# Performance work log

Hardware: AMD Instinct MI355X
Metric: run time of the kernel (lower is better)

## Reference

```python
import jax, jax.numpy as jnp
from jax import lax
import numpy as np

D_MODEL = 512
H = 4
DK = 128
DV = 256
DFF = 2048
N_LAYERS = 12
N_LOC = 100  # 10x10 patches

CONV_SPECS = [(8, 3, 3), (16, 8, 3), (32, 16, 3), (32, 32, 3), (64, 32, 3),
              (64, 64, 3), (128, 64, 3), (128, 128, 3), (256, 128, 3), (512, 256, 2)]
RELU_AFTER = [False, True, False, True, True, True, True, True, True, False]


def setup_inputs() -> dict:
    key = jax.random.key(0)
    keys = iter(jax.random.split(key, 64))

    def nrm(shape, scale=0.02):
        return jax.random.normal(next(keys), shape, dtype=jnp.float32) * scale

    inp = {"x": jax.random.normal(next(keys), (1, 3, 200, 200), dtype=jnp.float32)}
    for i, (o, c, k) in enumerate(CONV_SPECS, 1):
        inp[f"cw{i}"] = nrm((o, c, k, k))
        inp[f"cb{i}"] = nrm((o,))
    inp["Wq"] = nrm((N_LAYERS, H, D_MODEL, DK))
    inp["Wk"] = nrm((N_LAYERS, H, D_MODEL, DK))
    inp["Wv"] = nrm((N_LAYERS, H, D_MODEL, DV))
    inp["Wo"] = nrm((N_LAYERS, H * DV, D_MODEL))
    inp["W1"] = nrm((N_LAYERS, D_MODEL, DFF))
    inp["b1"] = nrm((N_LAYERS, DFF))
    inp["W2"] = nrm((N_LAYERS, DFF, D_MODEL))
    inp["b2"] = nrm((N_LAYERS, D_MODEL))
    return inp


def _extract_patches(x):
    # x: [1,3,200,200] -> 100 patches of [3,20,20], index = i*10 + j
    # patch(i,j) = x[:, :, 20j:20(j+1), 20i:20(i+1)]  (i=cols outer, j=rows inner)
    x = x.reshape(3, 10, 20, 10, 20)            # [c, j_blk, row, i_blk, col]
    return jnp.transpose(x, (3, 1, 0, 2, 4)).reshape(N_LOC, 3, 20, 20)


def _local_embed(patches, cws, cbs):
    h = patches  # [100,3,20,20]
    for w, b, r in zip(cws, cbs, RELU_AFTER):
        h = lax.conv_general_dilated(h, w, (1, 1), 'VALID',
                                     dimension_numbers=('NCHW', 'OIHW', 'NCHW'))
        h = h + b[None, :, None, None]
        if r:
            h = jax.nn.relu(h)
    return h.reshape(N_LOC, D_MODEL)  # spatial reduced to 1x1


def _location_embeddings():
    # createLocationEmbedding(i, j) only uses i (the column-block coordinate).
    pos = jnp.repeat(jnp.arange(0, 200, 20, dtype=jnp.float32), 10)  # [100]
    k = jnp.arange(256, dtype=jnp.float32)
    inv = jnp.power(jnp.float32(10000.0), 2.0 * k / 256.0)
    ang = pos[:, None] / inv[None, :]  # [100,256]
    return jnp.concatenate([jnp.sin(ang), jnp.cos(ang)], axis=1)  # [100,512]


def _encoder_layer(h, Wq, Wk, Wv, Wo, W1, b1, W2, b2):
    # Multi-head attention; NOTE: scale uses K.size(0) = n_locations (faithful quirk).
    scale = 1.0 / jnp.sqrt(jnp.float32(N_LOC))
    q = jnp.einsum('nd,hdk->hnk', h, Wq)
    k = jnp.einsum('nd,hdk->hnk', h, Wk)
    v = jnp.einsum('nd,hdv->hnv', h, Wv)
    s = jnp.einsum('hnk,hmk->hnm', q, k) * scale
    a = jax.nn.softmax(s, axis=-1)
    o = jnp.einsum('hnm,hmv->hnv', a, v)
    o = jnp.transpose(o, (1, 0, 2)).reshape(N_LOC, H * DV)
    h = h + o @ Wo
    h = h + (jax.nn.relu(h @ W1 + b1) @ W2 + b2)
    return h


def reference(x, cw1, cb1, cw2, cb2, cw3, cb3, cw4, cb4, cw5, cb5,
              cw6, cb6, cw7, cb7, cw8, cb8, cw9, cb9, cw10, cb10,
              Wq, Wk, Wv, Wo, W1, b1, W2, b2):
    cws = [cw1, cw2, cw3, cw4, cw5, cw6, cw7, cw8, cw9, cw10]
    cbs = [cb1, cb2, cb3, cb4, cb5, cb6, cb7, cb8, cb9, cb10]
    patches = _extract_patches(x)
    h = _local_embed(patches, cws, cbs)
    h = h + _location_embeddings()
    for n in range(N_LAYERS):
        h = _encoder_layer(h, Wq[n], Wk[n], Wv[n], Wo[n], W1[n], b1[n], W2[n], b2[n])
    return h
```

## Files before the change

kernel.cpp:

```cpp
#include <hip/hip_runtime.h>
#include <math.h>

#define NLOC 100

typedef __attribute__((ext_vector_type(8))) _Float16 half8;
typedef __attribute__((ext_vector_type(4))) float f32x4;

#define XP_OFF    0
#define H_OFF     160000
#define QKV_OFF   211200
#define OCAT_OFF  416000
#define FFN_OFF   467200
#define ACTA_OFF  569600
#define ACTB_OFF  889664
#define CWH_OFF   1209728
#define CW1_OFF   1765504
#define WQKVT_OFF 1765824
#define WOT_OFF   8057280
#define W1T_OFF   11203008
#define W2T_OFF   17494464

struct WPack { const float* w[9]; };

__global__ __launch_bounds__(256) void stage_xp(const float* __restrict__ x, float* __restrict__ xp)
{
    int idx = blockIdx.x*256 + threadIdx.x;
    if (idx >= 160000) return;
    int c = idx & 3;
    int idx2 = idx >> 2;
    int p = idx2 / 400;
    int rr = idx2 - p*400;
    int y = rr / 20, xx = rr - y*20;
    int pi = p/10, pj = p - pi*10;
    float v = 0.f;
    if (c < 3) v = x[c*40000 + (pj*20 + y)*200 + pi*20 + xx];
    xp[idx] = v;
}

__global__ __launch_bounds__(256) void cw1repack(const float* __restrict__ w, float* __restrict__ w4)
{
    int idx = threadIdx.x;
    if (idx >= 288) return;
    int c = idx & 3;
    int r = idx >> 2;
    int oc = r / 9, kk = r - oc*9;
    int ky = kk/3, kx = kk - ky*3;
    float v = 0.f;
    if (c < 3) v = w[((oc*3 + c)*3 + ky)*3 + kx];
    w4[idx] = v;
}

__global__ __launch_bounds__(256) void cwrepack(WPack wp, unsigned short* __restrict__ dst)
{
    const int Cin[9]  = {8,16,32,32,64,64,128,128,256};
    const int shift[9]= {3,4,5,5,6,6,7,7,8};
    const int KS[9]   = {3,3,3,3,3,3,3,3,2};
    const int Kpad[9] = {96,160,288,288,576,576,1152,1152,1024};
    const int off[10] = {0,1536,6656,15872,34304,71168,144896,292352,587264,1111552};
    const int total = 1111552;
    for (int i = blockIdx.x*blockDim.x + threadIdx.x; i < total; i += gridDim.x*blockDim.x) {
        int l = 0;
        while (i >= off[l+1]) ++l;
        int rem = i - off[l];
        int kp = Kpad[l];
        int oc = rem / kp;
        int k  = rem - oc*kp;
        int ci = Cin[l];
        int ic = k & (ci - 1);
        int kk = k >> shift[l];
        int ks = KS[l], k2 = ks*ks;
        float v = 0.f;
        if (kk < k2) {
            int ky = kk / ks, kx = kk - ky*ks;
            v = wp.w[l][((oc*ci + ic)*ks + ky)*ks + kx];
        }
        _Float16 hv = (_Float16)v;
        dst[i] = __builtin_bit_cast(unsigned short, hv);
    }
}

__global__ __launch_bounds__(256) void conv1k(const float4* __restrict__ xp4,
    const float4* __restrict__ w4, const float* __restrict__ bias, unsigned short* __restrict__ out)
{
    int idx = blockIdx.x*256 + threadIdx.x;
    if (idx >= 259200) return;
    int oc = idx & 7;
    int r = idx >> 3;
    int p = r / 324;
    int s = r - p*324;
    int sy = s / 18, sx = s - sy*18;
    const float4* ip = xp4 + (size_t)(p*20 + sy)*20 + sx;
    float acc = 0.f;
    #pragma unroll
    for (int ky = 0; ky < 3; ++ky)
        #pragma unroll
        for (int kx = 0; kx < 3; ++kx) {
            float4 iv = ip[ky*20 + kx];
            float4 wv = w4[oc*9 + ky*3 + kx];
            acc += iv.x*wv.x + iv.y*wv.y + iv.z*wv.z;
        }
    acc += bias[oc];
    _Float16 hv = (_Float16)acc;
    out[idx] = __builtin_bit_cast(unsigned short, hv);
}

template<int CIN, int COUT, int KS, int HIN, int WIN, int HOUT, int WOUT, int KPAD, int RELU, int LAST>
__global__ __launch_bounds__(256) void convM(const unsigned short* __restrict__ in,
    const unsigned short* __restrict__ wth, const float* __restrict__ bias,
    unsigned short* __restrict__ out, float* __restrict__ hout)
{
    constexpr int HW = HOUT*WOUT;
    constexpr int M = 100*HW;
    constexpr int MT = (M + 15)/16;
    constexpr int NT = COUT/16;
    int wave = threadIdx.x >> 6, lane = threadIdx.x & 63;
    int t = blockIdx.x*4 + wave;
    if (t >= MT*NT) return;
    int mt = t % MT, nt = t / MT;
    int mrow = lane & 15, quad = lane >> 4;
    int mg = mt*16 + mrow; if (mg >= M) mg = M - 1;
    int p = mg / HW, s = mg - p*HW;
    int sy = s / WOUT, sx = s - sy*WOUT;
    const unsigned short* ap = in + ((size_t)((p*HIN + sy)*WIN + sx))*CIN;
    const unsigned short* bp = wth + ((size_t)(nt*16 + mrow))*KPAD + quad*8;
    f32x4 acc = {0.f, 0.f, 0.f, 0.f};
    #pragma unroll
    for (int k0 = 0; k0 < KPAD; k0 += 32) {
        int k = k0 + quad*8;
        int kk = k / CIN; if (kk > KS*KS - 1) kk = KS*KS - 1;
        int ky = kk / KS, kx = kk - ky*KS;
        uint4 av = *(const uint4*)(ap + (ky*WIN + kx)*CIN + (k & (CIN-1)));
        uint4 bv = *(const uint4*)(bp + k0);
        acc = __builtin_amdgcn_mfma_f32_16x16x32_f16(
            __builtin_bit_cast(half8, av), __builtin_bit_cast(half8, bv), acc, 0, 0, 0);
    }
    int n = nt*16 + mrow;
    float bv = bias[n];
    #pragma unroll
    for (int r = 0; r < 4; ++r) {
        int m = mt*16 + quad*4 + r;
        if (m < M) {
            float v = acc[r] + bv;
            if (RELU) v = fmaxf(v, 0.f);
            if (LAST) {
                int pi = m / 10;
                float pos = 20.f * (float)pi;
                int dd = n & 255;
                float inv = powf(10000.f, (float)dd * (1.f/128.f));
                float ang = pos / inv;
                v += (n < 256) ? sinf(ang) : cosf(ang);
                hout[(size_t)m*512 + n] = v;
            } else {
                _Float16 hv = (_Float16)v;
                out[(size_t)m*COUT + n] = __builtin_bit_cast(unsigned short, hv);
            }
        }
    }
}

__global__ __launch_bounds__(256) void wtrans(
    const float* __restrict__ src, unsigned short* __restrict__ dst,
    int K, int N, int matsPerLayer, int dstLayerStride, int dstBase)
{
    __shared__ float t[32][33];
    int mz = blockIdx.z;
    int layer = mz / matsPerLayer;
    int mi = mz - layer*matsPerLayer;
    const float* s = src + (size_t)mz * K * N;
    unsigned short* d = dst + (size_t)layer*dstLayerStride + dstBase + (size_t)mi * N * K;
    int n0 = blockIdx.x*32, k0 = blockIdx.y*32;
    int tx = threadIdx.x & 31, ty = threadIdx.x >> 5;
    #pragma unroll
    for (int i = 0; i < 32; i += 8) t[ty + i][tx] = s[(size_t)(k0 + ty + i)*N + n0 + tx];
    __syncthreads();
    #pragma unroll
    for (int i = 0; i < 32; i += 8) {
        _Float16 hv = (_Float16)t[tx][ty + i];
        d[(size_t)(n0 + ty + i)*K + k0 + tx] = __builtin_bit_cast(unsigned short, hv);
    }
}

template<int ABITS, int RELU, int ATOMIC, int STOREH>
__global__ __launch_bounds__(256) void gemm16(
    const void* __restrict__ Av, int lda,
    const unsigned short* __restrict__ Bt, int K,
    const float* __restrict__ bias,
    float* __restrict__ C, unsigned short* __restrict__ Ch, int ldc,
    int kchunk)
{
    int lane = threadIdx.x & 63;
    int wave = threadIdx.x >> 6;
    int mrow = lane & 15, quad = lane >> 4;
    int n0 = blockIdx.x*64 + wave*16;
    int m0 = blockIdx.y*16;
    int arow = m0 + mrow; if (arow > 99) arow = 99;
    int k0 = blockIdx.z * kchunk;
    const unsigned short* bp = Bt + (size_t)(n0 + mrow)*K + quad*8 + k0;
    f32x4 acc = {0.f, 0.f, 0.f, 0.f};
    if (ABITS == 16) {
        const unsigned short* ap = (const unsigned short*)Av + (size_t)arow*lda + quad*8 + k0;
        for (int k = 0; k < kchunk; k += 32) {
            uint4 au = *(const uint4*)(ap + k);
            uint4 bu = *(const uint4*)(bp + k);
            acc = __builtin_amdgcn_mfma_f32_16x16x32_f16(
                __builtin_bit_cast(half8, au), __builtin_bit_cast(half8, bu), acc, 0, 0, 0);
        }
    } else {
        const float* ap = (const float*)Av + (size_t)arow*lda + quad*8 + k0;
        for (int k = 0; k < kchunk; k += 32) {
            float4 f0 = *(const float4*)(ap + k);
            float4 f1 = *(const float4*)(ap + k + 4);
            half8 af;
            af[0] = (_Float16)f0.x; af[1] = (_Float16)f0.y;
            af[2] = (_Float16)f0.z; af[3] = (_Float16)f0.w;
            af[4] = (_Float16)f1.x; af[5] = (_Float16)f1.y;
            af[6] = (_Float16)f1.z; af[7] = (_Float16)f1.w;
            uint4 bu = *(const uint4*)(bp + k);
            acc = __builtin_amdgcn_mfma_f32_16x16x32_f16(
                af, __builtin_bit_cast(half8, bu), acc, 0, 0, 0);
        }
    }
    int n = n0 + mrow;
    float bv = (bias != nullptr && blockIdx.z == 0) ? bias[n] : 0.f;
    #pragma unroll
    for (int r = 0; r < 4; ++r) {
        int row = m0 + quad*4 + r;
        if (row < 100) {
            float v = acc[r] + bv;
            if (RELU) v = fmaxf(v, 0.f);
            if (ATOMIC) atomicAdd(&C[(size_t)row*ldc + n], v);
            else if (C != nullptr) C[(size_t)row*ldc + n] = v;
            if (STOREH) {
                _Float16 hv = (_Float16)v;
                Ch[(size_t)row*ldc + n] = __builtin_bit_cast(unsigned short, hv);
            }
        }
    }
}

__global__ __launch_bounds__(256) void attn_kernel(
    const float* __restrict__ qkv, unsigned short* __restrict__ ocat)
{
    __shared__ float qr[128];
    __shared__ float p[100];
    __shared__ float red[2];
    int bx = blockIdx.x;
    int hh = bx / 100, nn = bx - hh*100;
    int t = threadIdx.x;
    if (t < 128) qr[t] = qkv[(size_t)nn*2048 + hh*128 + t];
    __syncthreads();
    float sv = 0.f;
    if (t < 100) {
        const float4* kp = (const float4*)(qkv + (size_t)t*2048 + 512 + hh*128);
        const float4* q4 = (const float4*)qr;
        float s0=0.f, s1=0.f, s2=0.f, s3=0.f;
        #pragma unroll 8
        for (int j = 0; j < 32; ++j) {
            float4 a = q4[j], b = kp[j];
            s0 += a.x*b.x; s1 += a.y*b.y; s2 += a.z*b.z; s3 += a.w*b.w;
        }
        sv = (s0+s1+s2+s3) * 0.1f;
        p[t] = sv;
    }
    __syncthreads();
    if (t < 64) {
        float m = fmaxf(p[t], (t+64 < 100) ? p[t+64] : -1e30f);
        for (int o = 32; o > 0; o >>= 1) m = fmaxf(m, __shfl_down(m, o));
        if (t == 0) red[0] = m;
    }
    __syncthreads();
    float mx = red[0];
    if (t < 100) p[t] = expf(sv - mx);
    __syncthreads();
    if (t < 64) {
        float s = p[t] + ((t+64 < 100) ? p[t+64] : 0.f);
        for (int o = 32; o > 0; o >>= 1) s += __shfl_down(s, o);
        if (t == 0) red[1] = s;
    }
    __syncthreads();
    float inv = 1.0f / red[1];
    const float* vp = qkv + 1024 + hh*256 + t;
    float acc = 0.f;
    #pragma unroll 4
    for (int m = 0; m < 100; ++m) acc += p[m] * vp[(size_t)m*2048];
    _Float16 hv = (_Float16)(acc * inv);
    ocat[(size_t)nn*1024 + hh*256 + t] = __builtin_bit_cast(unsigned short, hv);
}

__global__ __launch_bounds__(256) void copyk(const float* __restrict__ s, float* __restrict__ d, int n)
{
    int i = blockIdx.x*256 + threadIdx.x;
    if (i < n) d[i] = s[i];
}

extern "C" void kernel_launch(void* const* d_in, const int* in_sizes, int n_in,
                              void* d_out, int out_size, void* d_ws, size_t ws_size,
                              hipStream_t stream)
{
    const float* x = (const float*)d_in[0];
    const float* cw1 = (const float*)d_in[1];
    const float* cb[10];
    WPack wpk;
    for (int i = 0; i < 10; ++i) cb[i] = (const float*)d_in[2 + 2*i];
    for (int i = 0; i < 9; ++i)  wpk.w[i] = (const float*)d_in[3 + 2*i];
    const float* Wq = (const float*)d_in[21];
    const float* Wk = (const float*)d_in[22];
    const float* Wv = (const float*)d_in[23];
    const float* Wo = (const float*)d_in[24];
    const float* W1 = (const float*)d_in[25];
    const float* b1 = (const float*)d_in[26];
    const float* W2 = (const float*)d_in[27];
    const float* b2 = (const float*)d_in[28];

    float* ws = (float*)d_ws;
    float* xp  = ws + XP_OFF;
    float* h   = ws + H_OFF;
    float* qkv = ws + QKV_OFF;
    unsigned short* ocat = (unsigned short*)(ws + OCAT_OFF);
    unsigned short* ffn  = (unsigned short*)(ws + FFN_OFF);
    unsigned short* aA   = (unsigned short*)(ws + ACTA_OFF);
    unsigned short* aB   = (unsigned short*)(ws + ACTB_OFF);
    unsigned short* cwh  = (unsigned short*)(ws + CWH_OFF);
    float* cw14 = ws + CW1_OFF;
    unsigned short* wqkvt = (unsigned short*)(ws + WQKVT_OFF);
    unsigned short* wot   = (unsigned short*)(ws + WOT_OFF);
    unsigned short* w1t   = (unsigned short*)(ws + W1T_OFF);
    unsigned short* w2t   = (unsigned short*)(ws + W2T_OFF);

    cw1repack<<<2, 256, 0, stream>>>(cw1, cw14);
    cwrepack<<<2172, 256, 0, stream>>>(wpk, cwh);
    wtrans<<<dim3(4, 16, 48),  256, 0, stream>>>(Wq, wqkvt, 512, 128,  4, 2048*512, 0);
    wtrans<<<dim3(4, 16, 48),  256, 0, stream>>>(Wk, wqkvt, 512, 128,  4, 2048*512, 512*512);
    wtrans<<<dim3(8, 16, 48),  256, 0, stream>>>(Wv, wqkvt, 512, 256,  4, 2048*512, 1024*512);
    wtrans<<<dim3(16, 32, 12), 256, 0, stream>>>(Wo, wot,  1024, 512,  1, 512*1024, 0);
    wtrans<<<dim3(64, 16, 12), 256, 0, stream>>>(W1, w1t,   512, 2048, 1, 2048*512, 0);
    wtrans<<<dim3(16, 64, 12), 256, 0, stream>>>(W2, w2t,  2048, 512,  1, 512*2048, 0);

    stage_xp<<<625, 256, 0, stream>>>(x, xp);
    conv1k<<<1013, 256, 0, stream>>>((const float4*)xp, (const float4*)cw14, cb[0], aA);
    convM<8,  16, 3,18,18,16,16,  96,1,0><<<400, 256, 0, stream>>>(aA, cwh + 0,      cb[1], aB, nullptr);
    convM<16, 32, 3,16,16,14,14, 160,0,0><<<613, 256, 0, stream>>>(aB, cwh + 1536,   cb[2], aA, nullptr);
    convM<32, 32, 3,14,14,12,12, 288,1,0><<<450, 256, 0, stream>>>(aA, cwh + 6656,   cb[3], aB, nullptr);
    convM<32, 64, 3,12,12,10,10, 288,1,0><<<625, 256, 0, stream>>>(aB, cwh + 15872,  cb[4], aA, nullptr);
    convM<64, 64, 3,10,10, 8, 8, 576,1,0><<<400, 256, 0, stream>>>(aA, cwh + 34304,  cb[5], aB, nullptr);
    convM<64,128, 3, 8, 8, 6, 6, 576,1,0><<<450, 256, 0, stream>>>(aB, cwh + 71168,  cb[6], aA, nullptr);
    convM<128,128,3, 6, 6, 4, 4,1152,1,0><<<200, 256, 0, stream>>>(aA, cwh + 144896, cb[7], aB, nullptr);
    convM<128,256,3, 4, 4, 2, 2,1152,1,0><<<100, 256, 0, stream>>>(aB, cwh + 292352, cb[8], aA, nullptr);
    convM<256,512,2, 2, 2, 1, 1,1024,0,1><<<56,  256, 0, stream>>>(aA, cwh + 587264, cb[9], nullptr, h);

    for (int n = 0; n < 12; ++n) {
        const unsigned short* Bq  = wqkvt + (size_t)n * 2048 * 512;
        const unsigned short* Bo  = wot   + (size_t)n * 512 * 1024;
        const unsigned short* Bf1 = w1t   + (size_t)n * 2048 * 512;
        const unsigned short* Bf2 = w2t   + (size_t)n * 512 * 2048;
        gemm16<32,0,0,0><<<dim3(32, 7, 1), 256, 0, stream>>>(h, 512, Bq, 512,
            nullptr, qkv, nullptr, 2048, 512);
        attn_kernel<<<400, 256, 0, stream>>>(qkv, ocat);
        gemm16<16,0,1,0><<<dim3(8, 7, 4), 256, 0, stream>>>(ocat, 1024, Bo, 1024,
            nullptr, h, nullptr, 512, 256);
        gemm16<32,1,0,1><<<dim3(32, 7, 1), 256, 0, stream>>>(h, 512, Bf1, 512,
            b1 + (size_t)n*2048, nullptr, ffn, 2048, 512);
        gemm16<16,0,1,0><<<dim3(8, 7, 8), 256, 0, stream>>>(ffn, 2048, Bf2, 2048,
            b2 + (size_t)n*512, h, nullptr, 512, 256);
    }
    copyk<<<200, 256, 0, stream>>>(h, (float*)d_out, NLOC*512);
}
```

Before: 873.8 us.

## Fuse attention with output projection, merge weight transposes, and fold patch staging into conv1

Several changes land together. Attention and the Wo projection now run in one kernel per query row that reads fp32 Wo directly, which drops the Wo transpose and the ocat round trip. The five weight transposes are merged into one launch, and the patch staging kernel is folded into conv1, which now computes all 8 output channels per thread. The GEMM k-chunk becomes a template constant with unrolling, and the FFN2 split-K goes from 8 to 4; the fused Wo step trades MFMA for scalar fp32 FMAs over 100 blocks.

```diff
diff --git a/kernel.cpp b/kernel.cpp
--- a/kernel.cpp
+++ b/kernel.cpp
@@ -6,40 +6,23 @@
 typedef __attribute__((ext_vector_type(8))) _Float16 half8;
 typedef __attribute__((ext_vector_type(4))) float f32x4;
 
-#define XP_OFF    0
-#define H_OFF     160000
-#define QKV_OFF   211200
-#define OCAT_OFF  416000
-#define FFN_OFF   467200
-#define ACTA_OFF  569600
-#define ACTB_OFF  889664
-#define CWH_OFF   1209728
-#define CW1_OFF   1765504
-#define WQKVT_OFF 1765824
-#define WOT_OFF   8057280
-#define W1T_OFF   11203008
-#define W2T_OFF   17494464
+#define H_OFF     0
+#define QKV_OFF   51200
+#define FFN_OFF   256000
+#define ACTA_OFF  358400
+#define ACTB_OFF  678464
+#define CWH_OFF   998528
+#define CW1_OFF   1554304
+#define WQKVT_OFF 1554624
+#define W1T_OFF   7846080
+#define W2T_OFF   14137536
 
 struct WPack { const float* w[9]; };
-
-__global__ __launch_bounds__(256) void stage_xp(const float* __restrict__ x, float* __restrict__ xp)
+struct WTArgs { const float* src[5]; };
+
+__global__ __launch_bounds__(256) void cw1repack(const float* __restrict__ w, float* __restrict__ w4)
 {
     int idx = blockIdx.x*256 + threadIdx.x;
-    if (idx >= 160000) return;
-    int c = idx & 3;
-    int idx2 = idx >> 2;
-    int p = idx2 / 400;
-    int rr = idx2 - p*400;
-    int y = rr / 20, xx = rr - y*20;
-    int pi = p/10, pj = p - pi*10;
-    float v = 0.f;
-    if (c < 3) v = x[c*40000 + (pj*20 + y)*200 + pi*20 + xx];
-    xp[idx] = v;
-}
-
-__global__ __launch_bounds__(256) void cw1repack(const float* __restrict__ w, float* __restrict__ w4)
-{
-    int idx = threadIdx.x;
     if (idx >= 288) return;
     int c = idx & 3;
     int r = idx >> 2;
@@ -79,29 +62,79 @@
     }
 }
 
-__global__ __launch_bounds__(256) void conv1k(const float4* __restrict__ xp4,
+__global__ __launch_bounds__(256) void wtrans_all(WTArgs wa,
+    unsigned short* __restrict__ wqkvt, unsigned short* __restrict__ w1t,
+    unsigned short* __restrict__ w2t)
+{
+    const int pre[6]  = {0, 3072, 6144, 12288, 24576, 36864};
+    const int tX[5]   = {4, 4, 8, 64, 16};
+    const int tY[5]   = {16, 16, 16, 16, 64};
+    const int Kd[5]   = {512, 512, 512, 512, 2048};
+    const int Nd[5]   = {128, 128, 256, 2048, 512};
+    const int mpl[5]  = {4, 4, 4, 1, 1};
+    const int dls[5]  = {1048576, 1048576, 1048576, 1048576, 1048576};
+    const int dbase[5]= {0, 262144, 524288, 0, 0};
+    __shared__ float tsh[32][33];
+    int b = blockIdx.x;
+    int seg = 0;
+    while (b >= pre[seg+1]) ++seg;
+    int lb = b - pre[seg];
+    int tpm = tX[seg]*tY[seg];
+    int mz = lb / tpm;
+    int r = lb - mz*tpm;
+    int ty_ = r / tX[seg];
+    int tx_ = r - ty_*tX[seg];
+    int K = Kd[seg], N = Nd[seg];
+    int layer = mz / mpl[seg];
+    int mi = mz - layer*mpl[seg];
+    const float* s = wa.src[seg] + (size_t)mz * K * N;
+    unsigned short* base = (seg < 3) ? wqkvt : (seg == 3 ? w1t : w2t);
+    unsigned short* d = base + (size_t)layer*dls[seg] + dbase[seg] + (size_t)mi * N * K;
+    int n0 = tx_*32, k0 = ty_*32;
+    int lx = threadIdx.x & 31, ly = threadIdx.x >> 5;
+    #pragma unroll
+    for (int i = 0; i < 32; i += 8) tsh[ly + i][lx] = s[(size_t)(k0 + ly + i)*N + n0 + lx];
+    __syncthreads();
+    #pragma unroll
+    for (int i = 0; i < 32; i += 8) {
+        _Float16 hv = (_Float16)tsh[lx][ly + i];
+        d[(size_t)(n0 + ly + i)*K + k0 + lx] = __builtin_bit_cast(unsigned short, hv);
+    }
+}
+
+__global__ __launch_bounds__(256) void conv1k(const float* __restrict__ x,
     const float4* __restrict__ w4, const float* __restrict__ bias, unsigned short* __restrict__ out)
 {
     int idx = blockIdx.x*256 + threadIdx.x;
-    if (idx >= 259200) return;
-    int oc = idx & 7;
-    int r = idx >> 3;
-    int p = r / 324;
-    int s = r - p*324;
+    if (idx >= 32400) return;
+    int p = idx / 324;
+    int s = idx - p*324;
     int sy = s / 18, sx = s - sy*18;
-    const float4* ip = xp4 + (size_t)(p*20 + sy)*20 + sx;
-    float acc = 0.f;
+    int pi = p/10, pj = p - pi*10;
+    const float* xb = x + (pj*20 + sy)*200 + pi*20 + sx;
+    float acc[8];
+    #pragma unroll
+    for (int o = 0; o < 8; ++o) acc[o] = bias[o];
     #pragma unroll
     for (int ky = 0; ky < 3; ++ky)
         #pragma unroll
         for (int kx = 0; kx < 3; ++kx) {
-            float4 iv = ip[ky*20 + kx];
-            float4 wv = w4[oc*9 + ky*3 + kx];
-            acc += iv.x*wv.x + iv.y*wv.y + iv.z*wv.z;
-        }
-    acc += bias[oc];
-    _Float16 hv = (_Float16)acc;
-    out[idx] = __builtin_bit_cast(unsigned short, hv);
+            float r = xb[ky*200 + kx];
+            float g = xb[40000 + ky*200 + kx];
+            float bch = xb[80000 + ky*200 + kx];
+            #pragma unroll
+            for (int o = 0; o < 8; ++o) {
+                float4 wv = w4[o*9 + ky*3 + kx];
+                acc[o] += r*wv.x + g*wv.y + bch*wv.z;
+            }
+        }
+    unsigned short h8[8];
+    #pragma unroll
+    for (int o = 0; o < 8; ++o) {
+        _Float16 hv = (_Float16)acc[o];
+        h8[o] = __builtin_bit_cast(unsigned short, hv);
+    }
+    *(uint4*)(out + (size_t)idx*8) = *(const uint4*)h8;
 }
 
 template<int CIN, int COUT, int KS, int HIN, int WIN, int HOUT, int WOUT, int KPAD, int RELU, int LAST>
@@ -158,35 +191,12 @@
     }
 }
 
-__global__ __launch_bounds__(256) void wtrans(
-    const float* __restrict__ src, unsigned short* __restrict__ dst,
-    int K, int N, int matsPerLayer, int dstLayerStride, int dstBase)
-{
-    __shared__ float t[32][33];
-    int mz = blockIdx.z;
-    int layer = mz / matsPerLayer;
-    int mi = mz - layer*matsPerLayer;
-    const float* s = src + (size_t)mz * K * N;
-    unsigned short* d = dst + (size_t)layer*dstLayerStride + dstBase + (size_t)mi * N * K;
-    int n0 = blockIdx.x*32, k0 = blockIdx.y*32;
-    int tx = threadIdx.x & 31, ty = threadIdx.x >> 5;
-    #pragma unroll
-    for (int i = 0; i < 32; i += 8) t[ty + i][tx] = s[(size_t)(k0 + ty + i)*N + n0 + tx];
-    __syncthreads();
-    #pragma unroll
-    for (int i = 0; i < 32; i += 8) {
-        _Float16 hv = (_Float16)t[tx][ty + i];
-        d[(size_t)(n0 + ty + i)*K + k0 + tx] = __builtin_bit_cast(unsigned short, hv);
-    }
-}
-
-template<int ABITS, int RELU, int ATOMIC, int STOREH>
+template<int KCHUNK, int ABITS, int RELU, int ATOMIC, int STOREH>
 __global__ __launch_bounds__(256) void gemm16(
     const void* __restrict__ Av, int lda,
     const unsigned short* __restrict__ Bt, int K,
     const float* __restrict__ bias,
-    float* __restrict__ C, unsigned short* __restrict__ Ch, int ldc,
-    int kchunk)
+    float* __restrict__ C, unsigned short* __restrict__ Ch, int ldc)
 {
     int lane = threadIdx.x & 63;
     int wave = threadIdx.x >> 6;
@@ -194,12 +204,13 @@
     int n0 = blockIdx.x*64 + wave*16;
     int m0 = blockIdx.y*16;
     int arow = m0 + mrow; if (arow > 99) arow = 99;
-    int k0 = blockIdx.z * kchunk;
+    int k0 = blockIdx.z * KCHUNK;
     const unsigned short* bp = Bt + (size_t)(n0 + mrow)*K + quad*8 + k0;
     f32x4 acc = {0.f, 0.f, 0.f, 0.f};
     if (ABITS == 16) {
         const unsigned short* ap = (const unsigned short*)Av + (size_t)arow*lda + quad*8 + k0;
-        for (int k = 0; k < kchunk; k += 32) {
+        #pragma unroll 8
+        for (int k = 0; k < KCHUNK; k += 32) {
             uint4 au = *(const uint4*)(ap + k);
             uint4 bu = *(const uint4*)(bp + k);
             acc = __builtin_amdgcn_mfma_f32_16x16x32_f16(
@@ -207,7 +218,8 @@
         }
     } else {
         const float* ap = (const float*)Av + (size_t)arow*lda + quad*8 + k0;
-        for (int k = 0; k < kchunk; k += 32) {
+        #pragma unroll 8
+        for (int k = 0; k < KCHUNK; k += 32) {
             float4 f0 = *(const float4*)(ap + k);
             float4 f1 = *(const float4*)(ap + k + 4);
             half8 af;
@@ -238,53 +250,67 @@
     }
 }
 
-__global__ __launch_bounds__(256) void attn_kernel(
-    const float* __restrict__ qkv, unsigned short* __restrict__ ocat)
-{
-    __shared__ float qr[128];
-    __shared__ float p[100];
-    __shared__ float red[2];
-    int bx = blockIdx.x;
-    int hh = bx / 100, nn = bx - hh*100;
+__global__ __launch_bounds__(512) void attn_fused(
+    const float* __restrict__ qkv, const float* __restrict__ Wo,
+    float* __restrict__ h)
+{
+    __shared__ float qs[512];
+    __shared__ float sc[4][128];
+    __shared__ float os[1024];
+    __shared__ float sred[4];
+    int n = blockIdx.x;
     int t = threadIdx.x;
-    if (t < 128) qr[t] = qkv[(size_t)nn*2048 + hh*128 + t];
-    __syncthreads();
-    float sv = 0.f;
-    if (t < 100) {
-        const float4* kp = (const float4*)(qkv + (size_t)t*2048 + 512 + hh*128);
-        const float4* q4 = (const float4*)qr;
+    qs[t] = qkv[(size_t)n*2048 + t];
+    __syncthreads();
+    if (t < 400) {
+        int hh = t / 100, m = t - hh*100;
+        const float4* q4 = (const float4*)(qs + hh*128);
+        const float4* kp = (const float4*)(qkv + (size_t)m*2048 + 512 + hh*128);
         float s0=0.f, s1=0.f, s2=0.f, s3=0.f;
         #pragma unroll 8
         for (int j = 0; j < 32; ++j) {
             float4 a = q4[j], b = kp[j];
             s0 += a.x*b.x; s1 += a.y*b.y; s2 += a.z*b.z; s3 += a.w*b.w;
         }
-        sv = (s0+s1+s2+s3) * 0.1f;
-        p[t] = sv;
-    }
-    __syncthreads();
-    if (t < 64) {
-        float m = fmaxf(p[t], (t+64 < 100) ? p[t+64] : -1e30f);
+        sc[hh][m] = (s0+s1+s2+s3) * 0.1f;
+    }
+    __syncthreads();
+    int wv = t >> 6, ln = t & 63;
+    if (wv < 4) {
+        float v0 = (ln < 100)    ? sc[wv][ln]    : -1e30f;
+        float v1 = (ln+64 < 100) ? sc[wv][ln+64] : -1e30f;
+        float m = fmaxf(v0, v1);
         for (int o = 32; o > 0; o >>= 1) m = fmaxf(m, __shfl_down(m, o));
-        if (t == 0) red[0] = m;
-    }
-    __syncthreads();
-    float mx = red[0];
-    if (t < 100) p[t] = expf(sv - mx);
-    __syncthreads();
-    if (t < 64) {
-        float s = p[t] + ((t+64 < 100) ? p[t+64] : 0.f);
-        for (int o = 32; o > 0; o >>= 1) s += __shfl_down(s, o);
-        if (t == 0) red[1] = s;
-    }
-    __syncthreads();
-    float inv = 1.0f / red[1];
-    const float* vp = qkv + 1024 + hh*256 + t;
-    float acc = 0.f;
-    #pragma unroll 4
-    for (int m = 0; m < 100; ++m) acc += p[m] * vp[(size_t)m*2048];
-    _Float16 hv = (_Float16)(acc * inv);
-    ocat[(size_t)nn*1024 + hh*256 + t] = __builtin_bit_cast(unsigned short, hv);
+        m = __shfl(m, 0);
+        float e0 = expf(v0 - m);
+        float e1 = expf(v1 - m);
+        if (ln < 100)    sc[wv][ln]    = e0;
+        if (ln+64 < 100) sc[wv][ln+64] = e1;
+        float sm = ((ln < 100) ? e0 : 0.f) + ((ln+64 < 100) ? e1 : 0.f);
+        for (int o = 32; o > 0; o >>= 1) sm += __shfl_down(sm, o);
+        if (ln == 0) sred[wv] = 1.0f / sm;
+    }
+    __syncthreads();
+    {
+        int dv = t & 255;
+        int h0 = t >> 8;
+        float o0 = 0.f, o1 = 0.f;
+        const float* vb = qkv + 1024;
+        #pragma unroll 4
+        for (int m = 0; m < 100; ++m) {
+            const float* vr = vb + (size_t)m*2048 + dv;
+            o0 += sc[h0][m]   * vr[h0*256];
+            o1 += sc[h0+2][m] * vr[(h0+2)*256];
+        }
+        os[h0*256 + dv]     = o0 * sred[h0];
+        os[(h0+2)*256 + dv] = o1 * sred[h0+2];
+    }
+    __syncthreads();
+    float acc = h[(size_t)n*512 + t];
+    const float* wp = Wo + t;
+    #pragma unroll 8
+    for (int k = 0; k < 1024; ++k) acc += os[k] * wp[(size_t)k*512];
+    h[(size_t)n*512 + t] = acc;
 }
 
 __global__ __launch_bounds__(256) void copyk(const float* __restrict__ s, float* __restrict__ d, int n)
@@ -313,31 +339,24 @@
     const float* b2 = (const float*)d_in[28];
 
     float* ws = (float*)d_ws;
-    float* xp  = ws + XP_OFF;
     float* h   = ws + H_OFF;
     float* qkv = ws + QKV_OFF;
-    unsigned short* ocat = (unsigned short*)(ws + OCAT_OFF);
     unsigned short* ffn  = (unsigned short*)(ws + FFN_OFF);
     unsigned short* aA   = (unsigned short*)(ws + ACTA_OFF);
     unsigned short* aB   = (unsigned short*)(ws + ACTB_OFF);
     unsigned short* cwh  = (unsigned short*)(ws + CWH_OFF);
     float* cw14 = ws + CW1_OFF;
     unsigned short* wqkvt = (unsigned short*)(ws + WQKVT_OFF);
-    unsigned short* wot   = (unsigned short*)(ws + WOT_OFF);
     unsigned short* w1t   = (unsigned short*)(ws + W1T_OFF);
     unsigned short* w2t   = (unsigned short*)(ws + W2T_OFF);
 
     cw1repack<<<2, 256, 0, stream>>>(cw1, cw14);
     cwrepack<<<2172, 256, 0, stream>>>(wpk, cwh);
-    wtrans<<<dim3(4, 16, 48),  256, 0, stream>>>(Wq, wqkvt, 512, 128,  4, 2048*512, 0);
-    wtrans<<<dim3(4, 16, 48),  256, 0, stream>>>(Wk, wqkvt, 512, 128,  4, 2048*512, 512*512);
-    wtrans<<<dim3(8, 16, 48),  256, 0, stream>>>(Wv, wqkvt, 512, 256,  4, 2048*512, 1024*512);
-    wtrans<<<dim3(16, 32, 12), 256, 0, stream>>>(Wo, wot,  1024, 512,  1, 512*1024, 0);
-    wtrans<<<dim3(64, 16, 12), 256, 0, stream>>>(W1, w1t,   512, 2048, 1, 2048*512, 0);
-    wtrans<<<dim3(16, 64, 12), 256, 0, stream>>>(W2, w2t,  2048, 512,  1, 512*2048, 0);
-
-    stage_xp<<<625, 256, 0, stream>>>(x, xp);
-    conv1k<<<1013, 256, 0, stream>>>((const float4*)xp, (const float4*)cw14, cb[0], aA);
+    WTArgs wargs; wargs.src[0] = Wq; wargs.src[1] = Wk; wargs.src[2] = Wv;
+    wargs.src[3] = W1; wargs.src[4] = W2;
+    wtrans_all<<<36864, 256, 0, stream>>>(wargs, wqkvt, w1t, w2t);
+
+    conv1k<<<127, 256, 0, stream>>>(x, (const float4*)cw14, cb[0], aA);
     convM<8,  16, 3,18,18,16,16,  96,1,0><<<400, 256, 0, stream>>>(aA, cwh + 0,      cb[1], aB, nullptr);
     convM<16, 32, 3,16,16,14,14, 160,0,0><<<613, 256, 0, stream>>>(aB, cwh + 1536,   cb[2], aA, nullptr);
     convM<32, 32, 3,14,14,12,12, 288,1,0><<<450, 256, 0, stream>>>(aA, cwh + 6656,   cb[3], aB, nullptr);
@@ -350,18 +369,15 @@
 
     for (int n = 0; n < 12; ++n) {
         const unsigned short* Bq  = wqkvt + (size_t)n * 2048 * 512;
-        const unsigned short* Bo  = wot   + (size_t)n * 512 * 1024;
         const unsigned short* Bf1 = w1t   + (size_t)n * 2048 * 512;
         const unsigned short* Bf2 = w2t   + (size_t)n * 512 * 2048;
-        gemm16<32,0,0,0><<<dim3(32, 7, 1), 256, 0, stream>>>(h, 512, Bq, 512,
-            nullptr, qkv, nullptr, 2048, 512);
-        attn_kernel<<<400, 256, 0, stream>>>(qkv, ocat);
-        gemm16<16,0,1,0><<<dim3(8, 7, 4), 256, 0, stream>>>(ocat, 1024, Bo, 1024,
-            nullptr, h, nullptr, 512, 256);
-        gemm16<32,1,0,1><<<dim3(32, 7, 1), 256, 0, stream>>>(h, 512, Bf1, 512,
-            b1 + (size_t)n*2048, nullptr, ffn, 2048, 512);
-        gemm16<16,0,1,0><<<dim3(8, 7, 8), 256, 0, stream>>>(ffn, 2048, Bf2, 2048,
-            b2 + (size_t)n*512, h, nullptr, 512, 256);
+        gemm16<512,32,0,0,0><<<dim3(32, 7, 1), 256, 0, stream>>>(h, 512, Bq, 512,
+            nullptr, qkv, nullptr, 2048);
+        attn_fused<<<100, 512, 0, stream>>>(qkv, Wo + (size_t)n*1024*512, h);
+        gemm16<512,32,1,0,1><<<dim3(32, 7, 1), 256, 0, stream>>>(h, 512, Bf1, 512,
+            b1 + (size_t)n*2048, nullptr, ffn, 2048);
+        gemm16<512,16,0,1,0><<<dim3(8, 7, 4), 256, 0, stream>>>(ffn, 2048, Bf2, 2048,
+            b2 + (size_t)n*512, h, nullptr, 512);
     }
     copyk<<<200, 256, 0, stream>>>(h, (float*)d_out, NLOC*512);
 }
```

Result: slower. 1.643 ms (+88.1%).
